# Kernel optimization log

Hardware: AMD Instinct MI355X
Metric: run time of the kernel (lower is better)

Reference implementation:

```python
import jax, jax.numpy as jnp
import numpy as np

B, S, D_IN, D, H = 2, 2048, 1024, 1024, 16
HD = D // H

def setup_inputs() -> dict:
    key = jax.random.key(0)
    k1, k2, k3 = jax.random.split(key, 3)
    # xavier_uniform-style scale for weights
    lim_qkv = float(np.sqrt(6.0 / (D_IN + 3 * D)))
    lim_o = float(np.sqrt(6.0 / (D + D)))
    return {
        "x": jax.random.normal(k1, (B, S, D_IN), dtype=jnp.float32),
        "w_qkv": jax.random.uniform(k2, (3 * D, D_IN), dtype=jnp.float32, minval=-lim_qkv, maxval=lim_qkv),
        "b_qkv": jnp.zeros((3 * D,), dtype=jnp.float32),
        "w_o": jax.random.uniform(k3, (D, D), dtype=jnp.float32, minval=-lim_o, maxval=lim_o),
        "b_o": jnp.zeros((D,), dtype=jnp.float32),
    }

def reference(x, w_qkv, b_qkv, w_o, b_o):
    b, s, _ = x.shape
    # QKV projection: [B,S,3D]
    qkv = jnp.einsum("bsd,ed->bse", x, w_qkv) + b_qkv
    # [B,S,H,3*HD] -> [B,H,S,3*HD]
    qkv = qkv.reshape(b, s, H, 3 * HD).transpose(0, 2, 1, 3)
    q, k, v = jnp.split(qkv, 3, axis=-1)  # each [B,H,S,HD]
    scale = 1.0 / jnp.sqrt(jnp.asarray(HD, dtype=q.dtype))
    logits = jnp.einsum("bhqd,bhkd->bhqk", q, k) * scale  # [B,H,S,S]
    attn = jax.nn.softmax(logits, axis=-1)
    vals = jnp.einsum("bhqk,bhkd->bhqd", attn, v)  # [B,H,S,HD]
    vals = vals.transpose(0, 2, 1, 3).reshape(b, s, D)
    return jnp.einsum("bsd,ed->bse", vals, w_o) + b_o
```

## Files before the change

kernel.cpp:

```cpp
#include <hip/hip_runtime.h>
#include <hip/hip_bf16.h>
#include <math.h>

#define BATCH 2
#define SLEN  2048
#define DIN   1024
#define DMODEL 1024
#define NHEAD 16
#define HD    64
#define E3    3072

typedef unsigned short us;
typedef _Float16 f16;
typedef __attribute__((ext_vector_type(8))) _Float16 f16x8;
typedef __attribute__((ext_vector_type(8))) unsigned short us8;
typedef __attribute__((ext_vector_type(4))) unsigned short us4;
typedef __attribute__((ext_vector_type(4))) float f32x4;
typedef __attribute__((ext_vector_type(16))) float f32x16;
typedef __attribute__((ext_vector_type(4))) unsigned int u32x4;

#define QSCALE 0.18033688011112042f

__device__ __forceinline__ us f16bits(float x) {
    const f16 h = (f16)x;
    return __builtin_bit_cast(us, h);
}

__device__ __forceinline__ unsigned int pkrtz(float a, float b) {
    return __builtin_bit_cast(unsigned int, __builtin_amdgcn_cvt_pkrtz(a, b));
}

__device__ __forceinline__ void plswap(unsigned int& a, unsigned int& b) {
    asm volatile("v_permlane32_swap_b32 %0, %1" : "+v"(a), "+v"(b));
}

__device__ __forceinline__ void barrier_raw() {
    asm volatile("s_barrier" ::: "memory");
}

#define GLL16(g, l)                                                                     \
    __builtin_amdgcn_global_load_lds((const __attribute__((address_space(1))) unsigned int*)(g), \
                                     (__attribute__((address_space(3))) unsigned int*)(l), 16, 0, 0)

__global__ __launch_bounds__(256) void cvt3_f16(
    const float* __restrict__ x, us* __restrict__ ox, int nx,
    const float* __restrict__ wq, us* __restrict__ owq, int nq,
    const float* __restrict__ wo, us* __restrict__ owo)
{
    int i = (blockIdx.x * 256 + threadIdx.x) * 8;
    const float* s;
    us* o;
    if (i < nx)           { s = x;  o = ox; }
    else if (i < nx + nq) { s = wq; o = owq; i -= nx; }
    else                  { s = wo; o = owo; i -= nx + nq; }
    const float4 f0 = *(const float4*)&s[i];
    const float4 f1 = *(const float4*)&s[i + 4];
    const float v[8] = {f0.x, f0.y, f0.z, f0.w, f1.x, f1.y, f1.z, f1.w};
    us8 h;
#pragma unroll
    for (int j = 0; j < 8; ++j) h[j] = f16bits(v[j]);
    *(us8*)&o[i] = h;
}

#define GBK 64
#define GNT (DIN / GBK)

template <int BN, bool QKV_OUT>
__global__ __launch_bounds__(256) void gemm_db(
    const us* __restrict__ Am, const us* __restrict__ Bm,
    const float* __restrict__ bias, void* __restrict__ Cout,
    int M, int N, int K)
{
    constexpr int NJ  = BN / 32;
    constexpr int BGL = BN / 32;
    __shared__ __align__(16) us ldsA[2 * 128 * 64];
    __shared__ __align__(16) us ldsB[2 * BN * 64];

    const int t    = threadIdx.x;
    const int lane = t & 63;
    const int w    = t >> 6;
    const int ml   = lane & 15;
    const int quad = lane >> 4;
    const int msk  = ml & 7;
    const int wm   = w >> 1;
    const int wn   = w & 1;

    const int nbx = N / BN;
    const int nwg = (M >> 7) * nbx;
    int wg = blockIdx.y * nbx + blockIdx.x;
    wg = (wg & 7) * (nwg >> 3) + (wg >> 3);
    const int m0 = (wg / nbx) * 128;
    const int n0 = (wg % nbx) * BN;

    const int r8  = lane >> 3;
    const int xsw = ((lane & 7) ^ r8) * 8;
    const us* pA = Am + (size_t)(m0 + w * 32 + r8) * K + xsw;
    const int brow = (BN == 128) ? w * 32 : w * 16;
    const us* pB = Bm + (size_t)(n0 + brow + r8) * K + xsw;

#define STG_A(d, kk) do { _Pragma("unroll") for (int g = 0; g < 4; ++g) \
    GLL16(pA + (size_t)(8 * g) * K + (kk), &ldsA[(d) * 8192 + w * 2048 + g * 512]); } while (0)
#define STG_B(d, kk) do { _Pragma("unroll") for (int g = 0; g < BGL; ++g) \
    GLL16(pB + (size_t)(8 * g) * K + (kk), &ldsB[(d) * (BN * 64) + brow * 64 + g * 512]); } while (0)

#define LDA(d, mi, ks) __builtin_bit_cast(f16x8, *(const us8*)&ldsA[(d) * 8192 + (wm * 64 + (mi) * 16 + ml) * 64 + (((quad ^ msk) ^ ((ks) << 2)) * 8)])
#define LDB(d, nj, ks) __builtin_bit_cast(f16x8, *(const us8*)&ldsB[(d) * (BN * 64) + (wn * (BN / 2) + (nj) * 16 + ml) * 64 + (((quad ^ msk) ^ ((ks) << 2)) * 8)])

#define WAIT_BGL() do { if constexpr (BN == 128) asm volatile("s_waitcnt vmcnt(4)" ::: "memory"); \
                        else                     asm volatile("s_waitcnt vmcnt(2)" ::: "memory"); } while (0)

    f32x4 acc[4][NJ];
#pragma unroll
    for (int i = 0; i < 4; ++i)
#pragma unroll
        for (int j = 0; j < NJ; ++j) {
            acc[i][j][0] = 0.f; acc[i][j][1] = 0.f; acc[i][j][2] = 0.f; acc[i][j][3] = 0.f;
        }

    STG_A(0, 0); STG_B(0, 0);
    STG_B(1, GBK);
    WAIT_BGL();
    barrier_raw();

    for (int tt = 0; tt < GNT; ++tt) {
        const int d = tt & 1, e = d ^ 1;

        if (tt + 1 < GNT) STG_A(e, (tt + 1) * GBK);
        f16x8 bf[2][NJ];
#pragma unroll
        for (int ks = 0; ks < 2; ++ks)
#pragma unroll
            for (int nj = 0; nj < NJ; ++nj)
                bf[ks][nj] = LDB(d, nj, ks);
        f16x8 a0[2][2];
#pragma unroll
        for (int mi = 0; mi < 2; ++mi) {
            a0[mi][0] = LDA(d, mi, 0);
            a0[mi][1] = LDA(d, mi, 1);
        }
        __builtin_amdgcn_s_setprio(1);
#pragma unroll
        for (int ks = 0; ks < 2; ++ks)
#pragma unroll
            for (int nj = 0; nj < NJ; ++nj)
#pragma unroll
                for (int mi = 0; mi < 2; ++mi)
                    acc[mi][nj] = __builtin_amdgcn_mfma_f32_16x16x32_f16(a0[mi][ks], bf[ks][nj], acc[mi][nj], 0, 0, 0);
        __builtin_amdgcn_s_setprio(0);
        barrier_raw();

        if (tt + 2 < GNT) STG_B(d, (tt + 2) * GBK);
        f16x8 a1[2][2];
#pragma unroll
        for (int mi = 0; mi < 2; ++mi) {
            a1[mi][0] = LDA(d, mi + 2, 0);
            a1[mi][1] = LDA(d, mi + 2, 1);
        }
        __builtin_amdgcn_s_setprio(1);
#pragma unroll
        for (int ks = 0; ks < 2; ++ks)
#pragma unroll
            for (int nj = 0; nj < NJ; ++nj)
#pragma unroll
                for (int mi = 0; mi < 2; ++mi)
                    acc[mi + 2][nj] = __builtin_amdgcn_mfma_f32_16x16x32_f16(a1[mi][ks], bf[ks][nj], acc[mi + 2][nj], 0, 0, 0);
        __builtin_amdgcn_s_setprio(0);

        if (tt + 2 < GNT)      WAIT_BGL();
        else if (tt + 1 < GNT) asm volatile("s_waitcnt vmcnt(0)" ::: "memory");
        barrier_raw();
    }

    float bj[NJ], cs[NJ];
#pragma unroll
    for (int nj = 0; nj < NJ; ++nj) {
        const int col = n0 + wn * (BN / 2) + nj * 16 + ml;
        bj[nj] = bias[col];
        cs[nj] = (QKV_OUT && (col % 192) < 64) ? QSCALE : 1.0f;
    }
#pragma unroll
    for (int mi = 0; mi < 4; ++mi) {
#pragma unroll
        for (int r = 0; r < 4; ++r) {
            const size_t rowoff = (size_t)(m0 + wm * 64 + mi * 16 + quad * 4 + r) * N;
#pragma unroll
            for (int nj = 0; nj < NJ; ++nj) {
                const int col = n0 + wn * (BN / 2) + nj * 16 + ml;
                const float v = (acc[mi][nj][r] + bj[nj]) * cs[nj];
                if (QKV_OUT) ((us*)Cout)[rowoff + col] = f16bits(v);
                else         ((float*)Cout)[rowoff + col] = v;
            }
        }
    }
#undef STG_A
#undef STG_B
#undef LDA
#undef LDB
#undef WAIT_BGL
}

#define ABQ 128
#define ACH 64
#define NCH (SLEN / ACH)
#define NCH2 (NCH / 2)
#define LQA 72
#define OSTR 68

__global__ __launch_bounds__(512, 4) void attn_mfma(
    const us* __restrict__ qkvh, us* __restrict__ vals)
{
    __shared__ __align__(16) us smem[27648];
    us* const Qs = smem;
    us* const Ks = smem + 9216;
    us* const Vt = smem + 18432;

    const int t    = threadIdx.x;
    const int lane = t & 63;
    const int w    = t >> 6;
    const int sp   = w >> 2;
    const int wq4  = w & 3;
    const int t2   = t & 255;
    const int m32  = lane & 31;
    const int half = lane >> 5;

    const int wg  = blockIdx.x;
    const int s9  = wg >> 3;
    const int bh  = ((s9 >> 4) << 3) | (wg & 7);
    const int b   = bh >> 4;
    const int h   = bh & 15;
    const int q0  = (s9 & 15) * ABQ;

    const size_t base = (size_t)b * SLEN * E3;
    const int qoff = h * 192;

    {
        const int row = t >> 2;
        const int c0q = (t & 3) * 16;
        const us* g = &qkvh[base + (size_t)(q0 + row) * E3 + qoff + c0q];
        *(us8*)&Qs[row * LQA + c0q]     = *(const us8*)g;
        *(us8*)&Qs[row * LQA + c0q + 8] = *(const us8*)(g + 8);
    }
    __syncthreads();

    f16x8 aq[4];
#pragma unroll
    for (int s = 0; s < 4; ++s)
        aq[s] = __builtin_bit_cast(f16x8, *(const us8*)&Qs[(wq4 * 32 + m32) * LQA + half * 8 + 16 * s]);

    const int krA = t2 >> 2;
    const int ksA = (t2 & 3) * 16;
    const int k2  = t2 & 31;
    const int d0v = (t2 >> 5) * 8;

    us* const myK = Ks + sp * 4608;
    us* const myV = Vt + sp * 4608;
    const int cg0 = sp * NCH2;

    us8 kk0, kk1, vv0, vv1;
    {
        const us* gK = &qkvh[base + (size_t)(cg0 * ACH + krA) * E3 + qoff + 64 + ksA];
        kk0 = *(const us8*)gK; kk1 = *(const us8*)(gK + 8);
        const us* gV = &qkvh[base + (size_t)(cg0 * ACH + 2 * k2) * E3 + qoff + 128 + d0v];
        vv0 = *(const us8*)gV; vv1 = *(const us8*)(gV + E3);
    }

    f32x16 O[2];
#pragma unroll
    for (int dt = 0; dt < 2; ++dt)
#pragma unroll
        for (int r = 0; r < 16; ++r) O[dt][r] = 0.f;
    float lpart = 0.f;

    for (int c = 0; c < NCH2; ++c) {
        __syncthreads();
        *(us8*)&myK[krA * LQA + ksA]     = kk0;
        *(us8*)&myK[krA * LQA + ksA + 8] = kk1;
#pragma unroll
        for (int j = 0; j < 8; ++j) {
            const unsigned int pv = (unsigned int)vv0[j] | ((unsigned int)vv1[j] << 16);
            *(unsigned int*)&myV[(d0v + j) * LQA + 2 * k2] = pv;
        }
        __syncthreads();
        if (c + 1 < NCH2) {
            const int cg = cg0 + c + 1;
            const us* gK = &qkvh[base + (size_t)(cg * ACH + krA) * E3 + qoff + 64 + ksA];
            kk0 = *(const us8*)gK; kk1 = *(const us8*)(gK + 8);
            const us* gV = &qkvh[base + (size_t)(cg * ACH + 2 * k2) * E3 + qoff + 128 + d0v];
            vv0 = *(const us8*)gV; vv1 = *(const us8*)(gV + E3);
        }

        f16x8 pf[4];
#pragma unroll
        for (int kt = 0; kt < 2; ++kt) {
            f32x16 z;
#pragma unroll
            for (int r = 0; r < 16; ++r) z[r] = 0.f;
#pragma unroll
            for (int s = 0; s < 4; ++s) {
                const f16x8 ak = __builtin_bit_cast(f16x8, *(const us8*)&myK[(kt * 32 + m32) * LQA + half * 8 + 16 * s]);
                z = __builtin_amdgcn_mfma_f32_32x32x16_f16(ak, aq[s], z, 0, 0, 0);
            }
            float p[16];
#pragma unroll
            for (int r = 0; r < 16; ++r) {
                p[r] = __builtin_amdgcn_exp2f(z[r]);
                lpart += p[r];
            }
            unsigned int a0 = pkrtz(p[0],  p[1]),  a1 = pkrtz(p[2],  p[3]);
            unsigned int b0 = pkrtz(p[4],  p[5]),  b1 = pkrtz(p[6],  p[7]);
            plswap(a0, b0); plswap(a1, b1);
            pf[2 * kt] = __builtin_bit_cast(f16x8, (u32x4){a0, a1, b0, b1});
            unsigned int e0 = pkrtz(p[8],  p[9]),  e1 = pkrtz(p[10], p[11]);
            unsigned int f0 = pkrtz(p[12], p[13]), f1 = pkrtz(p[14], p[15]);
            plswap(e0, f0); plswap(e1, f1);
            pf[2 * kt + 1] = __builtin_bit_cast(f16x8, (u32x4){e0, e1, f0, f1});
        }

#pragma unroll
        for (int dt = 0; dt < 2; ++dt) {
#pragma unroll
            for (int s = 0; s < 4; ++s) {
                const f16x8 av = __builtin_bit_cast(f16x8, *(const us8*)&myV[(dt * 32 + m32) * LQA + half * 8 + 16 * s]);
                O[dt] = __builtin_amdgcn_mfma_f32_32x32x16_f16(av, pf[s], O[dt], 0, 0, 0);
            }
        }
    }

    const float l = lpart + __shfl_xor(lpart, 32);
    const int ql = wq4 * 32 + m32;

    __syncthreads();
    float* const Osc = (float*)(smem + 9216);
    float* const lsc = Osc + ABQ * OSTR;

    if (sp == 1) {
#pragma unroll
        for (int dt = 0; dt < 2; ++dt) {
#pragma unroll
            for (int g = 0; g < 4; ++g) {
                const f32x4 o4 = {O[dt][g * 4], O[dt][g * 4 + 1], O[dt][g * 4 + 2], O[dt][g * 4 + 3]};
                *(f32x4*)&Osc[ql * OSTR + dt * 32 + 8 * g + 4 * half] = o4;
            }
        }
        if (half == 0) lsc[ql] = l;
    }
    __syncthreads();
    if (sp == 0) {
        const float rl = 1.0f / (l + lsc[ql]);
        const int sq = q0 + ql;
        const size_t rowbase = (size_t)(b * SLEN + sq) * DMODEL + h * HD;
#pragma unroll
        for (int dt = 0; dt < 2; ++dt) {
#pragma unroll
            for (int g = 0; g < 4; ++g) {
                const f32x4 part = *(const f32x4*)&Osc[ql * OSTR + dt * 32 + 8 * g + 4 * half];
                us4 o4;
#pragma unroll
                for (int r2 = 0; r2 < 4; ++r2)
                    o4[r2] = f16bits((O[dt][g * 4 + r2] + part[r2]) * rl);
                *(us4*)&vals[rowbase + dt * 32 + 8 * g + 4 * half] = o4;
            }
        }
    }
}

extern "C" void kernel_launch(void* const* d_in, const int* in_sizes, int n_in,
                              void* d_out, int out_size, void* d_ws, size_t ws_size,
                              hipStream_t stream) {
    const float* x     = (const float*)d_in[0];
    const float* w_qkv = (const float*)d_in[1];
    const float* b_qkv = (const float*)d_in[2];
    const float* w_o   = (const float*)d_in[3];
    const float* b_o   = (const float*)d_in[4];
    float* out = (float*)d_out;

    const int M   = BATCH * SLEN;
    const int XN  = M * DIN;
    const int WQN = E3 * DIN;
    const int WON = DMODEL * DMODEL;
    const size_t QKVN = (size_t)BATCH * SLEN * E3;

    us* qkvh = (us*)d_ws;
    us* xh   = qkvh + QKVN;
    us* wq   = xh + XN;
    us* wo   = wq + WQN;

    cvt3_f16<<<dim3((XN + WQN + WON) / 2048), 256, 0, stream>>>(
        x, xh, XN, w_qkv, wq, WQN, w_o, wo);

    gemm_db<128, true><<<dim3(E3 / 128, M / 128), 256, 0, stream>>>(
        xh, wq, b_qkv, qkvh, M, E3, DIN);

    us* vals = xh;
    attn_mfma<<<dim3((SLEN / ABQ) * BATCH * NHEAD), 512, 0, stream>>>(qkvh, vals);

    gemm_db<64, false><<<dim3(DMODEL / 64, M / 128), 256, 0, stream>>>(
        vals, wo, b_o, out, M, DMODEL, DMODEL);
}
```

Measured before the change: 185.5 us.

## Double-buffer V tiles and reorder K/V staging in the attention loop

Adds a second V buffer in shared memory so the next chunk's V can be written while the current one is read. K is written after the QK^T stage behind a barrier, and global loads are issued two chunks ahead. The goal is to overlap LDS staging with MFMA work and to hide global load latency. The row-sum is split into four partial accumulators to shorten the dependency chain. LDS use per block grows from 27648 to 36864 halves, which may lower occupancy at 4 blocks of 512 threads per CU. The output scratch is moved to the start of shared memory.

```diff
diff --git a/kernel.cpp b/kernel.cpp
--- a/kernel.cpp
+++ b/kernel.cpp
@@ -209,7 +209,7 @@
 __global__ __launch_bounds__(512, 4) void attn_mfma(
     const us* __restrict__ qkvh, us* __restrict__ vals)
 {
-    __shared__ __align__(16) us smem[27648];
+    __shared__ __align__(16) us smem[36864];
     us* const Qs = smem;
     us* const Ks = smem + 9216;
     us* const Vt = smem + 18432;
@@ -233,6 +233,16 @@
     const size_t base = (size_t)b * SLEN * E3;
     const int qoff = h * 192;
 
+    const int krA = t2 >> 2;
+    const int ksA = (t2 & 3) * 16;
+    const int k2  = t2 & 31;
+    const int d0v = (t2 >> 5) * 8;
+
+    us* const myK  = Ks + sp * 4608;
+    us* const myV0 = Vt + sp * 4608;
+    us* const myV1 = Vt + 9216 + sp * 4608;
+    const int cg0 = sp * NCH2;
+
     {
         const int row = t >> 2;
         const int c0q = (t & 3) * 16;
@@ -240,21 +250,6 @@
         *(us8*)&Qs[row * LQA + c0q]     = *(const us8*)g;
         *(us8*)&Qs[row * LQA + c0q + 8] = *(const us8*)(g + 8);
     }
-    __syncthreads();
-
-    f16x8 aq[4];
-#pragma unroll
-    for (int s = 0; s < 4; ++s)
-        aq[s] = __builtin_bit_cast(f16x8, *(const us8*)&Qs[(wq4 * 32 + m32) * LQA + half * 8 + 16 * s]);
-
-    const int krA = t2 >> 2;
-    const int ksA = (t2 & 3) * 16;
-    const int k2  = t2 & 31;
-    const int d0v = (t2 >> 5) * 8;
-
-    us* const myK = Ks + sp * 4608;
-    us* const myV = Vt + sp * 4608;
-    const int cg0 = sp * NCH2;
 
     us8 kk0, kk1, vv0, vv1;
     {
@@ -263,30 +258,44 @@
         const us* gV = &qkvh[base + (size_t)(cg0 * ACH + 2 * k2) * E3 + qoff + 128 + d0v];
         vv0 = *(const us8*)gV; vv1 = *(const us8*)(gV + E3);
     }
+    *(us8*)&myK[krA * LQA + ksA]     = kk0;
+    *(us8*)&myK[krA * LQA + ksA + 8] = kk1;
+#pragma unroll
+    for (int j = 0; j < 8; ++j) {
+        const unsigned int pv = (unsigned int)vv0[j] | ((unsigned int)vv1[j] << 16);
+        *(unsigned int*)&myV0[(d0v + j) * LQA + 2 * k2] = pv;
+    }
+    if (1 < NCH2) {
+        const int cg = cg0 + 1;
+        const us* gK = &qkvh[base + (size_t)(cg * ACH + krA) * E3 + qoff + 64 + ksA];
+        kk0 = *(const us8*)gK; kk1 = *(const us8*)(gK + 8);
+        const us* gV = &qkvh[base + (size_t)(cg * ACH + 2 * k2) * E3 + qoff + 128 + d0v];
+        vv0 = *(const us8*)gV; vv1 = *(const us8*)(gV + E3);
+    }
+    __syncthreads();
+
+    f16x8 aq[4];
+#pragma unroll
+    for (int s = 0; s < 4; ++s)
+        aq[s] = __builtin_bit_cast(f16x8, *(const us8*)&Qs[(wq4 * 32 + m32) * LQA + half * 8 + 16 * s]);
 
     f32x16 O[2];
 #pragma unroll
     for (int dt = 0; dt < 2; ++dt)
 #pragma unroll
         for (int r = 0; r < 16; ++r) O[dt][r] = 0.f;
-    float lpart = 0.f;
+    float lp[4] = {0.f, 0.f, 0.f, 0.f};
 
     for (int c = 0; c < NCH2; ++c) {
-        __syncthreads();
-        *(us8*)&myK[krA * LQA + ksA]     = kk0;
-        *(us8*)&myK[krA * LQA + ksA + 8] = kk1;
-#pragma unroll
-        for (int j = 0; j < 8; ++j) {
-            const unsigned int pv = (unsigned int)vv0[j] | ((unsigned int)vv1[j] << 16);
-            *(unsigned int*)&myV[(d0v + j) * LQA + 2 * k2] = pv;
-        }
-        __syncthreads();
+        us* const Vrd = (c & 1) ? myV1 : myV0;
+        us* const Vwr = (c & 1) ? myV0 : myV1;
+
         if (c + 1 < NCH2) {
-            const int cg = cg0 + c + 1;
-            const us* gK = &qkvh[base + (size_t)(cg * ACH + krA) * E3 + qoff + 64 + ksA];
-            kk0 = *(const us8*)gK; kk1 = *(const us8*)(gK + 8);
-            const us* gV = &qkvh[base + (size_t)(cg * ACH + 2 * k2) * E3 + qoff + 128 + d0v];
-            vv0 = *(const us8*)gV; vv1 = *(const us8*)(gV + E3);
+#pragma unroll
+            for (int j = 0; j < 8; ++j) {
+                const unsigned int pv = (unsigned int)vv0[j] | ((unsigned int)vv1[j] << 16);
+                *(unsigned int*)&Vwr[(d0v + j) * LQA + 2 * k2] = pv;
+            }
         }
 
         f16x8 pf[4];
@@ -304,7 +313,7 @@
 #pragma unroll
             for (int r = 0; r < 16; ++r) {
                 p[r] = __builtin_amdgcn_exp2f(z[r]);
-                lpart += p[r];
+                lp[r & 3] += p[r];
             }
             unsigned int a0 = pkrtz(p[0],  p[1]),  a1 = pkrtz(p[2],  p[3]);
             unsigned int b0 = pkrtz(p[4],  p[5]),  b1 = pkrtz(p[6],  p[7]);
@@ -316,21 +325,38 @@
             pf[2 * kt + 1] = __builtin_bit_cast(f16x8, (u32x4){e0, e1, f0, f1});
         }
 
+        __syncthreads();
+
+        if (c + 1 < NCH2) {
+            *(us8*)&myK[krA * LQA + ksA]     = kk0;
+            *(us8*)&myK[krA * LQA + ksA + 8] = kk1;
+        }
+        if (c + 2 < NCH2) {
+            const int cg = cg0 + c + 2;
+            const us* gK = &qkvh[base + (size_t)(cg * ACH + krA) * E3 + qoff + 64 + ksA];
+            kk0 = *(const us8*)gK; kk1 = *(const us8*)(gK + 8);
+            const us* gV = &qkvh[base + (size_t)(cg * ACH + 2 * k2) * E3 + qoff + 128 + d0v];
+            vv0 = *(const us8*)gV; vv1 = *(const us8*)(gV + E3);
+        }
+
 #pragma unroll
         for (int dt = 0; dt < 2; ++dt) {
 #pragma unroll
             for (int s = 0; s < 4; ++s) {
-                const f16x8 av = __builtin_bit_cast(f16x8, *(const us8*)&myV[(dt * 32 + m32) * LQA + half * 8 + 16 * s]);
+                const f16x8 av = __builtin_bit_cast(f16x8, *(const us8*)&Vrd[(dt * 32 + m32) * LQA + half * 8 + 16 * s]);
                 O[dt] = __builtin_amdgcn_mfma_f32_32x32x16_f16(av, pf[s], O[dt], 0, 0, 0);
             }
         }
-    }
-
+
+        __syncthreads();
+    }
+
+    const float lpart = (lp[0] + lp[1]) + (lp[2] + lp[3]);
     const float l = lpart + __shfl_xor(lpart, 32);
     const int ql = wq4 * 32 + m32;
 
     __syncthreads();
-    float* const Osc = (float*)(smem + 9216);
+    float* const Osc = (float*)smem;
     float* const lsc = Osc + ABQ * OSTR;
 
     if (sp == 1) {
```

Result: no change. 186.6 us (+0.6%).
